# Performance work log

Hardware: AMD Instinct MI355X
Metric: run time of the kernel (lower is better)

## Reference

```python
import jax, jax.numpy as jnp
import numpy as np

RADIX = 16
INPUT_SIZE = 4096  # 16**3 -> 3 recursion levels
# residual flags per level, replicating the source quirk:
# level0: residual=True -> bool(True)=True, passes int(True)-1 = 0
# level1: residual=0    -> bool(0)=False,   passes int(0)-1   = -1
# level2: residual=-1   -> bool(-1)=True (negative ints are truthy)
RES_FLAGS = (True, False, True)


def _butterfly(x, weights, lins, res_flags):
    """Faithful vectorized translation of OptimisedRNNFFT.forward.

    x: (..., N); weights: list of per-level vectors (N, N/r, ...);
    lins: list of (radix, radix) matrices; res_flags: per-level residual bools.
    """
    n = x.shape[-1]
    chunk = n // RADIX
    if n > RADIX:
        # recurse on radix-sized chunks of the last dim
        xr = x.reshape(*x.shape[:-1], RADIX, chunk)
        y = _butterfly(xr, weights[1:], lins[1:], res_flags[1:])
        y = y.reshape(*x.shape[:-1], n)
    else:
        y = x  # Identity at the base level
    y = weights[0] * y                                   # elementwise weighting
    yb = y.reshape(*y.shape[:-1], RADIX, chunk)          # (..., radix, chunk)
    r = jnp.einsum('ij,...jc->...ic', lins[0], yb)       # radix x radix mix
    r = r.reshape(*y.shape[:-1], n)
    if res_flags[0]:
        r = r + x
    return r


def setup_inputs() -> dict:
    key = jax.random.key(0)
    k = jax.random.split(key, 8)
    x = jax.random.normal(k[0], (8192, INPUT_SIZE), dtype=jnp.float32)
    # per-level elementwise weights (torch init: ones/sqrt(N); randomized here)
    w0 = jax.random.normal(k[1], (4096,), dtype=jnp.float32) / np.sqrt(4096.0)
    w1 = jax.random.normal(k[2], (256,), dtype=jnp.float32) / np.sqrt(256.0)
    w2 = jax.random.normal(k[3], (16,), dtype=jnp.float32) / np.sqrt(16.0)
    # per-level radix x radix butterfly matrices (xavier-normal-ish)
    xav = np.sqrt(2.0 / (RADIX + RADIX))
    l0 = jax.random.normal(k[4], (RADIX, RADIX), dtype=jnp.float32) * xav
    l1 = jax.random.normal(k[5], (RADIX, RADIX), dtype=jnp.float32) * xav
    l2 = jax.random.normal(k[6], (RADIX, RADIX), dtype=jnp.float32) * xav
    return {"x": x, "w0": w0, "w1": w1, "w2": w2, "l0": l0, "l1": l1, "l2": l2}


def reference(x, w0, w1, w2, l0, l1, l2):
    return _butterfly(x, [w0, w1, w2], [l0, l1, l2], RES_FLAGS)
```

## Files before the change

kernel.cpp:

```cpp
#include <hip/hip_runtime.h>

#define N 4096

__device__ __forceinline__ int pad(int p) { return p + (p >> 4); }

__global__ __launch_bounds__(256, 4) void butterfly_kernel(
    const float* __restrict__ x,
    const float* __restrict__ w0, const float* __restrict__ w1, const float* __restrict__ w2,
    const float* __restrict__ l0, const float* __restrict__ l1, const float* __restrict__ l2,
    float* __restrict__ out)
{
    __shared__ float lds[N + (N >> 4)];
    const int t = threadIdx.x;
    const int row = blockIdx.x;
    const float* __restrict__ xr = x + (size_t)row * N;
    float* __restrict__ orow = out + (size_t)row * N;

    float v[16];
    const float4* xq = (const float4*)(xr + t * 16);
    #pragma unroll
    for (int q = 0; q < 4; ++q) {
        float4 f = xq[q];
        v[q*4+0] = f.x; v[q*4+1] = f.y; v[q*4+2] = f.z; v[q*4+3] = f.w;
    }

    float xw[16];
    #pragma unroll
    for (int j = 0; j < 16; ++j) xw[j] = w2[j] * v[j];
    float r2[16];
    #pragma unroll
    for (int i = 0; i < 16; ++i) {
        float acc = v[i];
        #pragma unroll
        for (int j = 0; j < 16; ++j) acc = fmaf(l2[i*16+j], xw[j], acc);
        r2[i] = acc;
    }

    #pragma unroll
    for (int k = 0; k < 16; ++k) lds[pad(t*16+k)] = r2[k];
    __syncthreads();

    const int b1 = t >> 4, c1 = t & 15;
    float y1[16];
    #pragma unroll
    for (int j = 0; j < 16; ++j)
        y1[j] = w1[j*16 + c1] * lds[pad(b1*256 + j*16 + c1)];
    float r1[16];
    #pragma unroll
    for (int i = 0; i < 16; ++i) {
        float acc = 0.f;
        #pragma unroll
        for (int j = 0; j < 16; ++j) acc = fmaf(l1[i*16+j], y1[j], acc);
        r1[i] = acc;
    }

    __syncthreads();
    #pragma unroll
    for (int i = 0; i < 16; ++i) lds[pad(b1*256 + i*16 + c1)] = r1[i];
    __syncthreads();

    float y0[16];
    #pragma unroll
    for (int j = 0; j < 16; ++j)
        y0[j] = w0[j*256 + t] * lds[pad(j*256 + t)];
    #pragma unroll
    for (int i = 0; i < 16; ++i) {
        float acc = 0.f;
        #pragma unroll
        for (int j = 0; j < 16; ++j) acc = fmaf(l0[i*16+j], y0[j], acc);
        orow[i*256 + t] = acc + xr[i*256 + t];
    }
}

extern "C" void kernel_launch(void* const* d_in, const int* in_sizes, int n_in,
                              void* d_out, int out_size, void* d_ws, size_t ws_size,
                              hipStream_t stream) {
    const float* x  = (const float*)d_in[0];
    const float* w0 = (const float*)d_in[1];
    const float* w1 = (const float*)d_in[2];
    const float* w2 = (const float*)d_in[3];
    const float* l0 = (const float*)d_in[4];
    const float* l1 = (const float*)d_in[5];
    const float* l2 = (const float*)d_in[6];
    float* out = (float*)d_out;
    const int rows = in_sizes[0] / N;
    butterfly_kernel<<<rows, 256, 0, stream>>>(x, w0, w1, w2, l0, l1, l2, out);
}
```

Baseline: 70.53 us.

## Process two rows per block with float2 LDS and hoisted weight/residual loads

Each block now handles two rows at once, storing interleaved float2 values in LDS so every shared-memory access and every scalar weight load (l0/l1/l2, w0/w1/w2) serves both rows. Weight columns and the residual x values are loaded before the barriers so their latency overlaps the synchronisation. The grid is halved and register pressure roughly doubles, which may limit occupancy under the 256x4 launch bound. LDS usage doubles to about 34 KB per block. An odd row count would drop the last row.

```diff
diff --git a/kernel.cpp b/kernel.cpp
--- a/kernel.cpp
+++ b/kernel.cpp
@@ -2,73 +2,114 @@
 
 #define N 4096
 
-__device__ __forceinline__ int pad(int p) { return p + (p >> 4); }
-
-__global__ __launch_bounds__(256, 4) void butterfly_kernel(
+__global__ __launch_bounds__(256, 4) void butterfly2_kernel(
     const float* __restrict__ x,
     const float* __restrict__ w0, const float* __restrict__ w1, const float* __restrict__ w2,
     const float* __restrict__ l0, const float* __restrict__ l1, const float* __restrict__ l2,
     float* __restrict__ out)
 {
-    __shared__ float lds[N + (N >> 4)];
+    __shared__ float2 lds[N + (N >> 4)];
     const int t = threadIdx.x;
-    const int row = blockIdx.x;
-    const float* __restrict__ xr = x + (size_t)row * N;
-    float* __restrict__ orow = out + (size_t)row * N;
+    const int b1 = t >> 4, c1 = t & 15;
+    const size_t row0 = (size_t)blockIdx.x * 2;
+    const float* __restrict__ xA = x + row0 * N;
+    const float* __restrict__ xB = xA + N;
+    float* __restrict__ oA = out + row0 * N;
+    float* __restrict__ oB = oA + N;
 
-    float v[16];
-    const float4* xq = (const float4*)(xr + t * 16);
-    #pragma unroll
-    for (int q = 0; q < 4; ++q) {
-        float4 f = xq[q];
-        v[q*4+0] = f.x; v[q*4+1] = f.y; v[q*4+2] = f.z; v[q*4+3] = f.w;
+    float vA[16], vB[16];
+    {
+        const float4* qA = (const float4*)(xA + t * 16);
+        const float4* qB = (const float4*)(xB + t * 16);
+        float4 fa0 = qA[0], fa1 = qA[1], fa2 = qA[2], fa3 = qA[3];
+        float4 fb0 = qB[0], fb1 = qB[1], fb2 = qB[2], fb3 = qB[3];
+        vA[0]=fa0.x; vA[1]=fa0.y; vA[2]=fa0.z; vA[3]=fa0.w;
+        vA[4]=fa1.x; vA[5]=fa1.y; vA[6]=fa1.z; vA[7]=fa1.w;
+        vA[8]=fa2.x; vA[9]=fa2.y; vA[10]=fa2.z; vA[11]=fa2.w;
+        vA[12]=fa3.x; vA[13]=fa3.y; vA[14]=fa3.z; vA[15]=fa3.w;
+        vB[0]=fb0.x; vB[1]=fb0.y; vB[2]=fb0.z; vB[3]=fb0.w;
+        vB[4]=fb1.x; vB[5]=fb1.y; vB[6]=fb1.z; vB[7]=fb1.w;
+        vB[8]=fb2.x; vB[9]=fb2.y; vB[10]=fb2.z; vB[11]=fb2.w;
+        vB[12]=fb3.x; vB[13]=fb3.y; vB[14]=fb3.z; vB[15]=fb3.w;
     }
 
-    float xw[16];
+    float xwA[16], xwB[16];
     #pragma unroll
-    for (int j = 0; j < 16; ++j) xw[j] = w2[j] * v[j];
-    float r2[16];
+    for (int j = 0; j < 16; ++j) {
+        float s = w2[j];
+        xwA[j] = s * vA[j];
+        xwB[j] = s * vB[j];
+    }
     #pragma unroll
     for (int i = 0; i < 16; ++i) {
-        float acc = v[i];
+        float a = vA[i], b = vB[i];
         #pragma unroll
-        for (int j = 0; j < 16; ++j) acc = fmaf(l2[i*16+j], xw[j], acc);
-        r2[i] = acc;
+        for (int j = 0; j < 16; ++j) {
+            float s = l2[i*16 + j];
+            a = fmaf(s, xwA[j], a);
+            b = fmaf(s, xwB[j], b);
+        }
+        lds[t*17 + i] = make_float2(a, b);
     }
 
+    float w1c[16];
     #pragma unroll
-    for (int k = 0; k < 16; ++k) lds[pad(t*16+k)] = r2[k];
+    for (int j = 0; j < 16; ++j) w1c[j] = w1[j*16 + c1];
+
     __syncthreads();
 
-    const int b1 = t >> 4, c1 = t & 15;
-    float y1[16];
+    float2 y1[16];
     #pragma unroll
-    for (int j = 0; j < 16; ++j)
-        y1[j] = w1[j*16 + c1] * lds[pad(b1*256 + j*16 + c1)];
-    float r1[16];
+    for (int j = 0; j < 16; ++j) {
+        float2 p = lds[b1*272 + j*17 + c1];
+        y1[j].x = w1c[j] * p.x;
+        y1[j].y = w1c[j] * p.y;
+    }
+    float r1A[16], r1B[16];
     #pragma unroll
     for (int i = 0; i < 16; ++i) {
-        float acc = 0.f;
+        float a = 0.f, b = 0.f;
         #pragma unroll
-        for (int j = 0; j < 16; ++j) acc = fmaf(l1[i*16+j], y1[j], acc);
-        r1[i] = acc;
+        for (int j = 0; j < 16; ++j) {
+            float s = l1[i*16 + j];
+            a = fmaf(s, y1[j].x, a);
+            b = fmaf(s, y1[j].y, b);
+        }
+        r1A[i] = a; r1B[i] = b;
     }
 
     __syncthreads();
     #pragma unroll
-    for (int i = 0; i < 16; ++i) lds[pad(b1*256 + i*16 + c1)] = r1[i];
+    for (int i = 0; i < 16; ++i)
+        lds[b1*272 + i*17 + c1] = make_float2(r1A[i], r1B[i]);
+
+    float w0c[16], xrA[16], xrB[16];
+    #pragma unroll
+    for (int j = 0; j < 16; ++j) w0c[j] = w0[j*256 + t];
+    #pragma unroll
+    for (int i = 0; i < 16; ++i) { xrA[i] = xA[i*256 + t]; xrB[i] = xB[i*256 + t]; }
+
     __syncthreads();
 
-    float y0[16];
+    const int tb = t + (t >> 4);
+    float2 y0[16];
     #pragma unroll
-    for (int j = 0; j < 16; ++j)
-        y0[j] = w0[j*256 + t] * lds[pad(j*256 + t)];
+    for (int j = 0; j < 16; ++j) {
+        float2 p = lds[j*272 + tb];
+        y0[j].x = w0c[j] * p.x;
+        y0[j].y = w0c[j] * p.y;
+    }
     #pragma unroll
     for (int i = 0; i < 16; ++i) {
-        float acc = 0.f;
+        float a = xrA[i], b = xrB[i];
         #pragma unroll
-        for (int j = 0; j < 16; ++j) acc = fmaf(l0[i*16+j], y0[j], acc);
-        orow[i*256 + t] = acc + xr[i*256 + t];
+        for (int j = 0; j < 16; ++j) {
+            float s = l0[i*16 + j];
+            a = fmaf(s, y0[j].x, a);
+            b = fmaf(s, y0[j].y, b);
+        }
+        oA[i*256 + t] = a;
+        oB[i*256 + t] = b;
     }
 }
 
@@ -84,5 +125,5 @@
     const float* l2 = (const float*)d_in[6];
     float* out = (float*)d_out;
     const int rows = in_sizes[0] / N;
-    butterfly_kernel<<<rows, 256, 0, stream>>>(x, w0, w1, w2, l0, l1, l2, out);
+    butterfly2_kernel<<<rows / 2, 256, 0, stream>>>(x, w0, w1, w2, l0, l1, l2, out);
 }
```

New measurement: 66.04 us. 6.4% less time.

## Drop block barriers by keeping level-1 exchange within a wavefront, add nontemporal stores

Applied to the files above, without the earlier changes.

The first two __syncthreads are removed. The level-2 to level-1 LDS exchange and the level-1 write-back only touch data owned by threads in the same 16-thread group, which sits inside one 64-wide wavefront, so a single barrier before level 0 is kept. The per-level weight loads are hoisted into registers before the barrier. The residual now seeds the accumulator, output uses nontemporal stores, and launch bounds ask for 8 blocks per CU. Correctness now depends on wave64 lockstep LDS ordering, and the occupancy hint may force register spills.

```diff
diff --git a/kernel.cpp b/kernel.cpp
--- a/kernel.cpp
+++ b/kernel.cpp
@@ -2,9 +2,7 @@
 
 #define N 4096
 
-__device__ __forceinline__ int pad(int p) { return p + (p >> 4); }
-
-__global__ __launch_bounds__(256, 4) void butterfly_kernel(
+__global__ __launch_bounds__(256, 8) void butterfly9_kernel(
     const float* __restrict__ x,
     const float* __restrict__ w0, const float* __restrict__ w1, const float* __restrict__ w2,
     const float* __restrict__ l0, const float* __restrict__ l1, const float* __restrict__ l2,
@@ -12,39 +10,39 @@
 {
     __shared__ float lds[N + (N >> 4)];
     const int t = threadIdx.x;
-    const int row = blockIdx.x;
-    const float* __restrict__ xr = x + (size_t)row * N;
-    float* __restrict__ orow = out + (size_t)row * N;
+    const int b1 = t >> 4, c1 = t & 15;
+    const float* __restrict__ xr = x + (size_t)blockIdx.x * N;
+    float* __restrict__ orow = out + (size_t)blockIdx.x * N;
 
     float v[16];
-    const float4* xq = (const float4*)(xr + t * 16);
-    #pragma unroll
-    for (int q = 0; q < 4; ++q) {
-        float4 f = xq[q];
-        v[q*4+0] = f.x; v[q*4+1] = f.y; v[q*4+2] = f.z; v[q*4+3] = f.w;
+    {
+        const float4* xq = (const float4*)(xr + t * 16);
+        #pragma unroll
+        for (int q = 0; q < 4; ++q) {
+            float4 f = xq[q];
+            v[q*4+0]=f.x; v[q*4+1]=f.y; v[q*4+2]=f.z; v[q*4+3]=f.w;
+        }
     }
 
     float xw[16];
     #pragma unroll
     for (int j = 0; j < 16; ++j) xw[j] = w2[j] * v[j];
-    float r2[16];
     #pragma unroll
     for (int i = 0; i < 16; ++i) {
         float acc = v[i];
         #pragma unroll
         for (int j = 0; j < 16; ++j) acc = fmaf(l2[i*16+j], xw[j], acc);
-        r2[i] = acc;
+        lds[t*17 + i] = acc;
     }
 
+    float w1c[16];
     #pragma unroll
-    for (int k = 0; k < 16; ++k) lds[pad(t*16+k)] = r2[k];
-    __syncthreads();
+    for (int j = 0; j < 16; ++j) w1c[j] = w1[j*16 + c1];
 
-    const int b1 = t >> 4, c1 = t & 15;
     float y1[16];
     #pragma unroll
     for (int j = 0; j < 16; ++j)
-        y1[j] = w1[j*16 + c1] * lds[pad(b1*256 + j*16 + c1)];
+        y1[j] = w1c[j] * lds[b1*272 + j*17 + c1];
     float r1[16];
     #pragma unroll
     for (int i = 0; i < 16; ++i) {
@@ -53,22 +51,27 @@
         for (int j = 0; j < 16; ++j) acc = fmaf(l1[i*16+j], y1[j], acc);
         r1[i] = acc;
     }
+    #pragma unroll
+    for (int i = 0; i < 16; ++i)
+        lds[b1*272 + i*17 + c1] = r1[i];
+
+    float w0c[16];
+    #pragma unroll
+    for (int j = 0; j < 16; ++j) w0c[j] = w0[j*256 + t];
 
     __syncthreads();
-    #pragma unroll
-    for (int i = 0; i < 16; ++i) lds[pad(b1*256 + i*16 + c1)] = r1[i];
-    __syncthreads();
 
+    const int tb = t + (t >> 4);
     float y0[16];
     #pragma unroll
     for (int j = 0; j < 16; ++j)
-        y0[j] = w0[j*256 + t] * lds[pad(j*256 + t)];
+        y0[j] = w0c[j] * lds[j*272 + tb];
     #pragma unroll
     for (int i = 0; i < 16; ++i) {
-        float acc = 0.f;
+        float acc = xr[i*256 + t];
         #pragma unroll
         for (int j = 0; j < 16; ++j) acc = fmaf(l0[i*16+j], y0[j], acc);
-        orow[i*256 + t] = acc + xr[i*256 + t];
+        __builtin_nontemporal_store(acc, &orow[i*256 + t]);
     }
 }
 
@@ -84,5 +87,5 @@
     const float* l2 = (const float*)d_in[6];
     float* out = (float*)d_out;
     const int rows = in_sizes[0] / N;
-    butterfly_kernel<<<rows, 256, 0, stream>>>(x, w0, w1, w2, l0, l1, l2, out);
+    butterfly9_kernel<<<rows, 256, 0, stream>>>(x, w0, w1, w2, l0, l1, l2, out);
 }
```

Result: slower. 92.97 us (+31.8%).
